# Kernel tuning notes

Hardware: AMD Instinct MI355X
Metric: run time of the kernel (lower is better)

The kernel has to match this reference:

```python
import jax, jax.numpy as jnp
import numpy as np

NUM_EMBEDDINGS = 512
EMBEDDING_DIM = 64
BETA = 0.25


def setup_inputs() -> dict:
    key = jax.random.key(0)
    k1, k2 = jax.random.split(key)
    latent_z = jax.random.normal(k1, (32, EMBEDDING_DIM, 64, 64), dtype=jnp.float32)
    # nn.Embedding init: uniform(-1/K, 1/K)
    scale = 1.0 / NUM_EMBEDDINGS
    embedding = jax.random.uniform(k2, (NUM_EMBEDDINGS, EMBEDDING_DIM), dtype=jnp.float32,
                                   minval=-scale, maxval=scale)
    return {"latent_z": latent_z, "embedding": embedding}


def reference(latent_z, embedding):
    # [B, C, H, W] -> [B, H, W, C]
    z = jnp.transpose(latent_z, (0, 2, 3, 1))
    B, H, W, D = z.shape
    flat_z = z.reshape(-1, D)  # [N, D]

    # squared L2 distances via expansion: ||z||^2 + ||e||^2 - 2 z.e
    dist = (jnp.sum(flat_z ** 2, axis=1, keepdims=True)
            + jnp.sum(embedding ** 2, axis=1)
            - 2.0 * flat_z @ embedding.T)  # [N, K]

    idx = jnp.argmin(dist, axis=1)  # [N]
    encodings = jax.nn.one_hot(idx, NUM_EMBEDDINGS, dtype=flat_z.dtype)  # [N, K]

    # gather codes (same math as one_hot @ embedding)
    quantized = embedding[idx].reshape(B, H, W, D)

    quant_loss = (jnp.mean((jax.lax.stop_gradient(quantized) - z) ** 2)
                  + BETA * jnp.mean((quantized - jax.lax.stop_gradient(z)) ** 2))

    # straight-through estimator
    quantized_st = z + jax.lax.stop_gradient(quantized - z)

    mean_enc = jnp.mean(encodings, axis=0)
    perplexity = jnp.exp(-jnp.sum(mean_enc * jnp.log(mean_enc + 1e-10)))

    quantized_out = jnp.transpose(quantized_st, (0, 3, 1, 2))  # back to [B, C, H, W]
    return quant_loss, quantized_out, perplexity, encodings, idx[:, None]
```

## Files before the change

### kernel.cpp

```cpp
#include <hip/hip_runtime.h>
#include <math.h>

#define NPIX   131072
#define KCODES 512
#define DIM    64
#define HW     4096
#define CHW    262144

#define O_Q    1ll
#define O_PERP 8388609ll
#define O_ENC  8388610ll
#define O_IDX  75497474ll


__device__ __forceinline__ float np_sumsq64(const float (&x)[64]) {
#pragma clang fp contract(off)
  float r0 = x[0]*x[0], r1 = x[1]*x[1], r2 = x[2]*x[2], r3 = x[3]*x[3];
  float r4 = x[4]*x[4], r5 = x[5]*x[5], r6 = x[6]*x[6], r7 = x[7]*x[7];
#pragma unroll
  for (int i = 8; i < 64; i += 8) {
    r0 += x[i+0]*x[i+0];
    r1 += x[i+1]*x[i+1];
    r2 += x[i+2]*x[i+2];
    r3 += x[i+3]*x[i+3];
    r4 += x[i+4]*x[i+4];
    r5 += x[i+5]*x[i+5];
    r6 += x[i+6]*x[i+6];
    r7 += x[i+7]*x[i+7];
  }
  return ((r0+r1)+(r2+r3))+((r4+r5)+(r6+r7));
}

__global__ void vq_prep(const float* __restrict__ emb, float* __restrict__ ws) {
  const int t = threadIdx.x;
  if (t == 0) ws[0] = 0.0f;
  ((unsigned*)ws)[1 + t] = 0u;
  float x[64];
  const float* e = emb + t * DIM;
#pragma unroll
  for (int d = 0; d < 64; ++d) x[d] = e[d];
  ws[513 + t] = np_sumsq64(x);
}

__global__ __launch_bounds__(256)
__attribute__((amdgpu_waves_per_eu(4, 4)))
void vq_main(
    const float* __restrict__ z, const float* __restrict__ emb,
    float* __restrict__ out, float* __restrict__ ws)
{
  __shared__ float ET_s[16 * 256];
  __shared__ float z_l[64 * 64];
  __shared__ float esq_l[512];
  __shared__ float zsq_l[64];
  __shared__ int   ridx_l[64];
  __shared__ float wsum[4];

  const int t   = threadIdx.x;
  const int ci  = t & 31;
  const int pi  = t >> 5;
  const int blk = blockIdx.x;
  const int n0  = blk * 64;
  const int b   = n0 >> 12;
  const int hw0 = n0 & 4095;
  const float* zg = z + (size_t)b * CHW + hw0;

  esq_l[t]       = ws[513 + t];
  esq_l[t + 256] = ws[769 + t];

  {
    const int i     = t & 15;
    const int dbase = t >> 4;
#pragma unroll
    for (int r = 0; r < 4; ++r) {
      const int d = dbase + 16 * r;
      const float4 v = *(const float4*)(zg + (size_t)d * HW + 4 * i);
      *(float4*)&z_l[d * 64 + 4 * i] = v;
    }
  }
  __syncthreads();

  if (t < 64) {
    float x[64];
#pragma unroll
    for (int d = 0; d < 64; ++d) x[d] = z_l[d * 64 + t];
    zsq_l[t] = np_sumsq64(x);
  }

  float bd[8];
  int   bk[8];
#pragma unroll
  for (int j = 0; j < 8; ++j) { bd[j] = INFINITY; bk[j] = 0; }

  for (int H = 0; H < 2; ++H) {
    float acc[8][8];
#pragma unroll
    for (int j = 0; j < 8; ++j)
#pragma unroll
      for (int c = 0; c < 8; ++c) acc[j][c] = 0.0f;

    for (int s = 0; s < 4; ++s) {
      __syncthreads();
      {
        const float* er = emb + (size_t)(256 * H + t) * 64 + 16 * s;
        const float4 v0 = *(const float4*)(er + 0);
        const float4 v1 = *(const float4*)(er + 4);
        const float4 v2 = *(const float4*)(er + 8);
        const float4 v3 = *(const float4*)(er + 12);
        float tmp[16] = {v0.x, v0.y, v0.z, v0.w, v1.x, v1.y, v1.z, v1.w,
                         v2.x, v2.y, v2.z, v2.w, v3.x, v3.y, v3.z, v3.w};
#pragma unroll
        for (int dl = 0; dl < 16; ++dl) ET_s[dl * 256 + t] = tmp[dl];
      }
      __syncthreads();

#pragma unroll 2
      for (int dl = 0; dl < 16; ++dl) {
        const float* zp = &z_l[(16 * s + dl) * 64 + 8 * pi];
        const float4 za0 = *(const float4*)(zp + 0);
        const float4 za1 = *(const float4*)(zp + 4);
        const float* ep = &ET_s[dl * 256 + 4 * ci];
        const float4 e0 = *(const float4*)(ep + 0);
        const float4 e1 = *(const float4*)(ep + 128);
        const float zr[8] = {za0.x, za0.y, za0.z, za0.w,
                             za1.x, za1.y, za1.z, za1.w};
        const float er_[8] = {e0.x, e0.y, e0.z, e0.w,
                              e1.x, e1.y, e1.z, e1.w};
#pragma unroll
        for (int j = 0; j < 8; ++j)
#pragma unroll
          for (int c = 0; c < 8; ++c)
            acc[j][c] = fmaf(zr[j], er_[c], acc[j][c]);
      }
    }

#pragma unroll
    for (int q = 0; q < 2; ++q)
#pragma unroll
      for (int r = 0; r < 4; ++r) {
        const int k = 256 * H + 128 * q + 4 * ci + r;
        const float eq = esq_l[k];
#pragma unroll
        for (int j = 0; j < 8; ++j) {
          const float dist = (zsq_l[8 * pi + j] + eq) - 2.0f * acc[j][4 * q + r];
          if (dist < bd[j]) { bd[j] = dist; bk[j] = k; }
        }
      }
  }

#pragma unroll
  for (int m = 16; m >= 1; m >>= 1) {
#pragma unroll
    for (int j = 0; j < 8; ++j) {
      const float od = __shfl_xor(bd[j], m, 64);
      const int   ok = __shfl_xor(bk[j], m, 64);
      if (od < bd[j] || (od == bd[j] && ok < bk[j])) { bd[j] = od; bk[j] = ok; }
    }
  }
  if (ci == 0) {
#pragma unroll
    for (int j = 0; j < 8; ++j) ridx_l[8 * pi + j] = bk[j];
  }
  __syncthreads();

  if (t < 64) {
    const int k = ridx_l[t];
    out[O_IDX + n0 + t] = (float)k;
    atomicAdd((unsigned*)ws + 1 + k, 1u);
  }

  {
    const int px = t & 63;
    const int dq = t >> 6;
    const int k  = ridx_l[px];
    const float* e0 = emb + ((size_t)k << 6);
    float* q0 = out + O_Q + (size_t)b * CHW + hw0 + px;
    float lsum = 0.0f;
#pragma unroll
    for (int j = 0; j < 16; ++j) {
      const int d = dq * 16 + j;
      const float ev = e0[d];
      const float df = ev - z_l[d * 64 + px];
      lsum = fmaf(df, df, lsum);
      q0[(size_t)d * HW] = ev;
    }
#pragma unroll
    for (int off = 32; off > 0; off >>= 1) lsum += __shfl_down(lsum, off, 64);
    if ((t & 63) == 0) wsum[t >> 6] = lsum;
  }
  __syncthreads();
  if (t == 0) atomicAdd(ws, (wsum[0] + wsum[1]) + (wsum[2] + wsum[3]));

  float2* enc = (float2*)(out + O_ENC) + (size_t)n0 * 256;
  for (int i = t; i < 64 * 256; i += 256) {
    const int r  = i >> 8;
    const int c2 = i & 255;
    const int bv = ridx_l[r];
    float2 v = make_float2(0.0f, 0.0f);
    if ((bv >> 1) == c2) {
      if (bv & 1) v.y = 1.0f; else v.x = 1.0f;
    }
    enc[i] = v;
  }
}

__global__ void vq_fin(float* __restrict__ out, const float* __restrict__ ws) {
  __shared__ float red[8];
  const int t = threadIdx.x;
  const unsigned* counts = (const unsigned*)ws + 1;
  const float p = (float)counts[t] * (1.0f / 131072.0f);
  float h = p * logf(p + 1e-10f);
#pragma unroll
  for (int off = 32; off > 0; off >>= 1) h += __shfl_down(h, off, 64);
  if ((t & 63) == 0) red[t >> 6] = h;
  __syncthreads();
  if (t == 0) {
    float H = 0.0f;
#pragma unroll
    for (int w = 0; w < 8; ++w) H += red[w];
    out[O_PERP] = expf(-H);
    out[0] = 1.25f * ws[0] * (1.0f / 8388608.0f);
  }
}

extern "C" void kernel_launch(void* const* d_in, const int* in_sizes, int n_in,
                              void* d_out, int out_size, void* d_ws, size_t ws_size,
                              hipStream_t stream) {
  const float* z   = (const float*)d_in[0];
  const float* emb = (const float*)d_in[1];
  float* out = (float*)d_out;
  float* ws  = (float*)d_ws;

  vq_prep<<<1, 512, 0, stream>>>(emb, ws);
  vq_main<<<2048, 256, 0, stream>>>(z, emb, out, ws);
  vq_fin<<<1, 512, 0, stream>>>(out, ws);
}
```

Before: 450.3 us.

## Double block size, prefetch codebook chunks, interleave one-hot zero stores with compute

Each block now handles 128 pixels with 512 threads, so every codebook chunk staged in shared memory is reused across twice as many pixels. The next embedding chunk is prefetched into registers before the current chunk's FMA loop runs, hiding global load latency. The large one-hot encodings write is split into zero-fill stores spread across the eight compute stages, followed by a scatter of the single 1.0 per row, so the write traffic overlaps the distance computation. The cost is more shared memory and register pressure per block, and the 1.0 store must land after the zero stores from other threads.

```diff
diff --git a/kernel.cpp b/kernel.cpp
--- a/kernel.cpp
+++ b/kernel.cpp
@@ -42,47 +42,54 @@
   ws[513 + t] = np_sumsq64(x);
 }
 
-__global__ __launch_bounds__(256)
-__attribute__((amdgpu_waves_per_eu(4, 4)))
+__global__ __launch_bounds__(512, 4)
 void vq_main(
     const float* __restrict__ z, const float* __restrict__ emb,
     float* __restrict__ out, float* __restrict__ ws)
 {
   __shared__ float ET_s[16 * 256];
-  __shared__ float z_l[64 * 64];
+  __shared__ float z_l[64 * 128];
   __shared__ float esq_l[512];
-  __shared__ float zsq_l[64];
-  __shared__ int   ridx_l[64];
-  __shared__ float wsum[4];
+  __shared__ float zsq_l[128];
+  __shared__ int   ridx_l[128];
+  __shared__ float wsum[8];
 
   const int t   = threadIdx.x;
   const int ci  = t & 31;
   const int pi  = t >> 5;
   const int blk = blockIdx.x;
-  const int n0  = blk * 64;
+  const int n0  = blk * 128;
   const int b   = n0 >> 12;
   const int hw0 = n0 & 4095;
   const float* zg = z + (size_t)b * CHW + hw0;
 
-  esq_l[t]       = ws[513 + t];
-  esq_l[t + 256] = ws[769 + t];
+  esq_l[t] = ws[513 + t];
 
   {
-    const int i     = t & 15;
-    const int dbase = t >> 4;
+    const int i     = t & 31;
+    const int dbase = t >> 5;
 #pragma unroll
     for (int r = 0; r < 4; ++r) {
       const int d = dbase + 16 * r;
-      const float4 v = *(const float4*)(zg + (size_t)d * HW + 4 * i);
-      *(float4*)&z_l[d * 64 + 4 * i] = v;
-    }
-  }
-  __syncthreads();
-
-  if (t < 64) {
+      *(float4*)&z_l[d * 128 + 4 * i] = *(const float4*)(zg + (size_t)d * HW + 4 * i);
+    }
+  }
+
+  const int ec = t & 255;
+  const int eh = t >> 8;
+  float4 p0, p1;
+  {
+    const float* er = emb + (size_t)ec * 64 + 8 * eh;
+    p0 = *(const float4*)(er + 0);
+    p1 = *(const float4*)(er + 4);
+  }
+
+  __syncthreads();
+
+  if (t < 128) {
     float x[64];
 #pragma unroll
-    for (int d = 0; d < 64; ++d) x[d] = z_l[d * 64 + t];
+    for (int d = 0; d < 64; ++d) x[d] = z_l[d * 128 + t];
     zsq_l[t] = np_sumsq64(x);
   }
 
@@ -90,6 +97,9 @@
   int   bk[8];
 #pragma unroll
   for (int j = 0; j < 8; ++j) { bd[j] = INFINITY; bk[j] = 0; }
+
+  float2* encb = (float2*)(out + O_ENC) + (size_t)n0 * 256;
+  const float2 zz = make_float2(0.0f, 0.0f);
 
   for (int H = 0; H < 2; ++H) {
     float acc[8][8];
@@ -101,21 +111,30 @@
     for (int s = 0; s < 4; ++s) {
       __syncthreads();
       {
-        const float* er = emb + (size_t)(256 * H + t) * 64 + 16 * s;
-        const float4 v0 = *(const float4*)(er + 0);
-        const float4 v1 = *(const float4*)(er + 4);
-        const float4 v2 = *(const float4*)(er + 8);
-        const float4 v3 = *(const float4*)(er + 12);
-        float tmp[16] = {v0.x, v0.y, v0.z, v0.w, v1.x, v1.y, v1.z, v1.w,
-                         v2.x, v2.y, v2.z, v2.w, v3.x, v3.y, v3.z, v3.w};
-#pragma unroll
-        for (int dl = 0; dl < 16; ++dl) ET_s[dl * 256 + t] = tmp[dl];
+        const float tmp[8] = {p0.x, p0.y, p0.z, p0.w, p1.x, p1.y, p1.z, p1.w};
+#pragma unroll
+        for (int dl = 0; dl < 8; ++dl) ET_s[(8 * eh + dl) * 256 + ec] = tmp[dl];
       }
       __syncthreads();
+
+      if (!(H == 1 && s == 3)) {
+        const int nH = (s < 3) ? H : 1;
+        const int ns = (s < 3) ? (s + 1) : 0;
+        const float* er = emb + (size_t)(256 * nH + ec) * 64 + 16 * ns + 8 * eh;
+        p0 = *(const float4*)(er + 0);
+        p1 = *(const float4*)(er + 4);
+      }
+
+      {
+        const int batch = 4 * H + s;
+#pragma unroll
+        for (int u = 0; u < 8; ++u)
+          encb[(size_t)batch * 4096 + u * 512 + t] = zz;
+      }
 
 #pragma unroll 2
       for (int dl = 0; dl < 16; ++dl) {
-        const float* zp = &z_l[(16 * s + dl) * 64 + 8 * pi];
+        const float* zp = &z_l[(16 * s + dl) * 128 + 8 * pi];
         const float4 za0 = *(const float4*)(zp + 0);
         const float4 za1 = *(const float4*)(zp + 4);
         const float* ep = &ET_s[dl * 256 + 4 * ci];
@@ -162,15 +181,16 @@
   }
   __syncthreads();
 
-  if (t < 64) {
+  if (t < 128) {
     const int k = ridx_l[t];
     out[O_IDX + n0 + t] = (float)k;
     atomicAdd((unsigned*)ws + 1 + k, 1u);
+    out[O_ENC + (size_t)(n0 + t) * 512 + k] = 1.0f;
   }
 
   {
-    const int px = t & 63;
-    const int dq = t >> 6;
+    const int px = t & 127;
+    const int dq = t >> 7;
     const int k  = ridx_l[px];
     const float* e0 = emb + ((size_t)k << 6);
     float* q0 = out + O_Q + (size_t)b * CHW + hw0 + px;
@@ -179,7 +199,7 @@
     for (int j = 0; j < 16; ++j) {
       const int d = dq * 16 + j;
       const float ev = e0[d];
-      const float df = ev - z_l[d * 64 + px];
+      const float df = ev - z_l[d * 128 + px];
       lsum = fmaf(df, df, lsum);
       q0[(size_t)d * HW] = ev;
     }
@@ -188,19 +208,9 @@
     if ((t & 63) == 0) wsum[t >> 6] = lsum;
   }
   __syncthreads();
-  if (t == 0) atomicAdd(ws, (wsum[0] + wsum[1]) + (wsum[2] + wsum[3]));
-
-  float2* enc = (float2*)(out + O_ENC) + (size_t)n0 * 256;
-  for (int i = t; i < 64 * 256; i += 256) {
-    const int r  = i >> 8;
-    const int c2 = i & 255;
-    const int bv = ridx_l[r];
-    float2 v = make_float2(0.0f, 0.0f);
-    if ((bv >> 1) == c2) {
-      if (bv & 1) v.y = 1.0f; else v.x = 1.0f;
-    }
-    enc[i] = v;
-  }
+  if (t == 0)
+    atomicAdd(ws, ((wsum[0] + wsum[1]) + (wsum[2] + wsum[3])) +
+                  ((wsum[4] + wsum[5]) + (wsum[6] + wsum[7])));
 }
 
 __global__ void vq_fin(float* __restrict__ out, const float* __restrict__ ws) {
@@ -231,6 +241,6 @@
   float* ws  = (float*)d_ws;
 
   vq_prep<<<1, 512, 0, stream>>>(emb, ws);
-  vq_main<<<2048, 256, 0, stream>>>(z, emb, out, ws);
+  vq_main<<<1024, 512, 0, stream>>>(z, emb, out, ws);
   vq_fin<<<1, 512, 0, stream>>>(out, ws);
 }
```

Result: faster. 426.0 us (-5.4%).

## Interleave one-hot zero stores with distance GEMM and read transposed codebook from global

Applied to the files above, without the earlier changes.

vq_prep now also writes a transposed copy of the codebook into the workspace, and vq_main reads its codebook operands straight from that global copy. This drops the per-stage LDS staging and its barriers. The large one-hot encoding zero-fill is spread across the GEMM loop as nontemporal double stores, so the write traffic overlaps with compute, and a single 1.0 is scattered per pixel afterwards. The quantized output stores become nontemporal, and the occupancy hint changes to launch_bounds(256,4). The risks are extra global/L2 load pressure in the inner loop and a possible ordering hazard between the zero stores and the later 1.0 writes from other threads.

```diff
diff --git a/kernel.cpp b/kernel.cpp
--- a/kernel.cpp
+++ b/kernel.cpp
@@ -6,12 +6,14 @@
 #define DIM    64
 #define HW     4096
 #define CHW    262144
+#define NBLK   2048
 
 #define O_Q    1ll
 #define O_PERP 8388609ll
 #define O_ENC  8388610ll
 #define O_IDX  75497474ll
 
+#define WS_EMBT 1280
 
 __device__ __forceinline__ float np_sumsq64(const float (&x)[64]) {
 #pragma clang fp contract(off)
@@ -40,15 +42,34 @@
 #pragma unroll
   for (int d = 0; d < 64; ++d) x[d] = e[d];
   ws[513 + t] = np_sumsq64(x);
-}
-
-__global__ __launch_bounds__(256)
-__attribute__((amdgpu_waves_per_eu(4, 4)))
+#pragma unroll
+  for (int d = 0; d < 64; ++d) ws[WS_EMBT + d * 512 + t] = x[d];
+}
+
+__device__ __forceinline__ void dist_phase(int Hh, int ci, int pi,
+                                           const float (&acc)[8][8],
+                                           const float* __restrict__ esq_l,
+                                           const float* __restrict__ zsq_l,
+                                           float (&bd)[8], int (&bk)[8]) {
+#pragma unroll
+  for (int q = 0; q < 2; ++q)
+#pragma unroll
+    for (int r = 0; r < 4; ++r) {
+      const int k = 256 * Hh + 128 * q + 4 * ci + r;
+      const float eq = esq_l[k];
+#pragma unroll
+      for (int j = 0; j < 8; ++j) {
+        const float dist = (zsq_l[8 * pi + j] + eq) - 2.0f * acc[j][4 * q + r];
+        if (dist < bd[j]) { bd[j] = dist; bk[j] = k; }
+      }
+    }
+}
+
+__global__ __launch_bounds__(256, 4)
 void vq_main(
     const float* __restrict__ z, const float* __restrict__ emb,
     float* __restrict__ out, float* __restrict__ ws)
 {
-  __shared__ float ET_s[16 * 256];
   __shared__ float z_l[64 * 64];
   __shared__ float esq_l[512];
   __shared__ float zsq_l[64];
@@ -62,7 +83,8 @@
   const int n0  = blk * 64;
   const int b   = n0 >> 12;
   const int hw0 = n0 & 4095;
-  const float* zg = z + (size_t)b * CHW + hw0;
+  const float* zg   = z + (size_t)b * CHW + hw0;
+  const float* embT = ws + WS_EMBT;
 
   esq_l[t]       = ws[513 + t];
   esq_l[t + 256] = ws[769 + t];
@@ -73,8 +95,7 @@
 #pragma unroll
     for (int r = 0; r < 4; ++r) {
       const int d = dbase + 16 * r;
-      const float4 v = *(const float4*)(zg + (size_t)d * HW + 4 * i);
-      *(float4*)&z_l[d * 64 + 4 * i] = v;
+      *(float4*)&z_l[d * 64 + 4 * i] = *(const float4*)(zg + (size_t)d * HW + 4 * i);
     }
   }
   __syncthreads();
@@ -85,66 +106,50 @@
     for (int d = 0; d < 64; ++d) x[d] = z_l[d * 64 + t];
     zsq_l[t] = np_sumsq64(x);
   }
+  __syncthreads();
 
   float bd[8];
   int   bk[8];
 #pragma unroll
   for (int j = 0; j < 8; ++j) { bd[j] = INFINITY; bk[j] = 0; }
 
+  double* encd = (double*)(out + O_ENC) + (size_t)n0 * 256;
+
   for (int H = 0; H < 2; ++H) {
+    const float* eTH = embT + 256 * H + 4 * ci;
     float acc[8][8];
 #pragma unroll
     for (int j = 0; j < 8; ++j)
 #pragma unroll
       for (int c = 0; c < 8; ++c) acc[j][c] = 0.0f;
 
-    for (int s = 0; s < 4; ++s) {
-      __syncthreads();
+    for (int ds = 0; ds < 4; ++ds) {
       {
-        const float* er = emb + (size_t)(256 * H + t) * 64 + 16 * s;
-        const float4 v0 = *(const float4*)(er + 0);
-        const float4 v1 = *(const float4*)(er + 4);
-        const float4 v2 = *(const float4*)(er + 8);
-        const float4 v3 = *(const float4*)(er + 12);
-        float tmp[16] = {v0.x, v0.y, v0.z, v0.w, v1.x, v1.y, v1.z, v1.w,
-                         v2.x, v2.y, v2.z, v2.w, v3.x, v3.y, v3.z, v3.w};
-#pragma unroll
-        for (int dl = 0; dl < 16; ++dl) ET_s[dl * 256 + t] = tmp[dl];
+        const int batch = 4 * H + ds;
+#pragma unroll
+        for (int u = 0; u < 8; ++u)
+          __builtin_nontemporal_store(0.0, encd + (size_t)batch * 2048 + u * 256 + t);
       }
-      __syncthreads();
-
-#pragma unroll 2
-      for (int dl = 0; dl < 16; ++dl) {
-        const float* zp = &z_l[(16 * s + dl) * 64 + 8 * pi];
+#pragma unroll
+      for (int dq = 0; dq < 16; ++dq) {
+        const int dl = 16 * ds + dq;
+        const float4 e0 = *(const float4*)(eTH + dl * 512);
+        const float4 e1 = *(const float4*)(eTH + dl * 512 + 128);
+        const float* zp = &z_l[dl * 64 + 8 * pi];
         const float4 za0 = *(const float4*)(zp + 0);
         const float4 za1 = *(const float4*)(zp + 4);
-        const float* ep = &ET_s[dl * 256 + 4 * ci];
-        const float4 e0 = *(const float4*)(ep + 0);
-        const float4 e1 = *(const float4*)(ep + 128);
         const float zr[8] = {za0.x, za0.y, za0.z, za0.w,
                              za1.x, za1.y, za1.z, za1.w};
-        const float er_[8] = {e0.x, e0.y, e0.z, e0.w,
-                              e1.x, e1.y, e1.z, e1.w};
+        const float er[8] = {e0.x, e0.y, e0.z, e0.w,
+                             e1.x, e1.y, e1.z, e1.w};
 #pragma unroll
         for (int j = 0; j < 8; ++j)
 #pragma unroll
           for (int c = 0; c < 8; ++c)
-            acc[j][c] = fmaf(zr[j], er_[c], acc[j][c]);
+            acc[j][c] = fmaf(zr[j], er[c], acc[j][c]);
       }
     }
-
-#pragma unroll
-    for (int q = 0; q < 2; ++q)
-#pragma unroll
-      for (int r = 0; r < 4; ++r) {
-        const int k = 256 * H + 128 * q + 4 * ci + r;
-        const float eq = esq_l[k];
-#pragma unroll
-        for (int j = 0; j < 8; ++j) {
-          const float dist = (zsq_l[8 * pi + j] + eq) - 2.0f * acc[j][4 * q + r];
-          if (dist < bd[j]) { bd[j] = dist; bk[j] = k; }
-        }
-      }
+    dist_phase(H, ci, pi, acc, esq_l, zsq_l, bd, bk);
   }
 
 #pragma unroll
@@ -166,6 +171,7 @@
     const int k = ridx_l[t];
     out[O_IDX + n0 + t] = (float)k;
     atomicAdd((unsigned*)ws + 1 + k, 1u);
+    out[O_ENC + (size_t)(n0 + t) * 512 + k] = 1.0f;
   }
 
   {
@@ -181,7 +187,7 @@
       const float ev = e0[d];
       const float df = ev - z_l[d * 64 + px];
       lsum = fmaf(df, df, lsum);
-      q0[(size_t)d * HW] = ev;
+      __builtin_nontemporal_store(ev, q0 + (size_t)d * HW);
     }
 #pragma unroll
     for (int off = 32; off > 0; off >>= 1) lsum += __shfl_down(lsum, off, 64);
@@ -189,18 +195,6 @@
   }
   __syncthreads();
   if (t == 0) atomicAdd(ws, (wsum[0] + wsum[1]) + (wsum[2] + wsum[3]));
-
-  float2* enc = (float2*)(out + O_ENC) + (size_t)n0 * 256;
-  for (int i = t; i < 64 * 256; i += 256) {
-    const int r  = i >> 8;
-    const int c2 = i & 255;
-    const int bv = ridx_l[r];
-    float2 v = make_float2(0.0f, 0.0f);
-    if ((bv >> 1) == c2) {
-      if (bv & 1) v.y = 1.0f; else v.x = 1.0f;
-    }
-    enc[i] = v;
-  }
 }
 
 __global__ void vq_fin(float* __restrict__ out, const float* __restrict__ ws) {
@@ -231,6 +225,6 @@
   float* ws  = (float*)d_ws;
 
   vq_prep<<<1, 512, 0, stream>>>(emb, ws);
-  vq_main<<<2048, 256, 0, stream>>>(z, emb, out, ws);
+  vq_main<<<NBLK, 256, 0, stream>>>(z, emb, out, ws);
   vq_fin<<<1, 512, 0, stream>>>(out, ws);
 }
```

New measurement: 604.9 us. 34.3% more time.
